# Optimization experiments

Hardware: AMD Instinct MI355X
Metric: run time of the kernel (lower is better)

The kernel has to match this reference:

```python
import jax, jax.numpy as jnp
import numpy as np


def setup_inputs() -> dict:
    key = jax.random.key(0)
    k1, k2, k3 = jax.random.split(key, 3)
    return {
        "x": jax.random.normal(k1, (1, 64, 28, 28), dtype=jnp.float32),
        "w1": jax.random.normal(k2, (128, 32, 3, 3, 2), dtype=jnp.float32),  # weights[0]
        "w2": jax.random.normal(k3, (64, 3, 2), dtype=jnp.float32),          # weights[1]
    }


def reference(x, w1, w2):
    # Stage 1: first unfold + einsum == depthwise size-3 conv along W (pad 1),
    # producing 2 taps (k) per channel.
    xr = x.reshape(64, 28, 28)                      # (j, m=H, n=W)
    xp = jnp.pad(xr, ((0, 0), (0, 0), (1, 1)))      # zero-pad W by 1
    # t3[j, m, i, n] = xp[j, m, n + i]  (i = kernel offset 0..2)
    t3 = jnp.stack([xp[:, :, i:i + 28] for i in range(3)], axis=2)  # (64,28,3,28)
    t4 = jnp.einsum('jmin,jik->jmnk', t3, w2)       # (64,28,28,2)

    # Stage 2: pairwise channel-sum 64 -> 32
    t5 = t4.reshape(32, 2, 28, 28, 2).sum(axis=1)   # (l=32, h=28, w=28, k=2)

    # Stage 3: the two remaining unfolds + final einsum == standard 3x3 conv,
    # pad 1, in_channels = (l,k) = 64, out_channels = 128.
    inp = jnp.transpose(t5, (0, 3, 1, 2)).reshape(1, 64, 28, 28)       # NCHW, C=(l,k)
    w = jnp.transpose(w1, (0, 1, 4, 2, 3)).reshape(128, 64, 3, 3)      # OIHW, I=(l,m)
    y = jax.lax.conv_general_dilated(
        inp, w, window_strides=(1, 1), padding=((1, 1), (1, 1)),
        dimension_numbers=('NCHW', 'OIHW', 'NCHW'))
    return y  # (1, 128, 28, 28)
```

## Files before the change

### kernel.cpp

```cpp
#include <hip/hip_runtime.h>
#include <hip/hip_bf16.h>

__global__ __launch_bounds__(256, 2) void fused_kernel(
    const float* __restrict__ x,
    const float* __restrict__ w1,
    const float* __restrict__ w2,
    float* __restrict__ y)
{
    __shared__ __align__(16) float sA[64 * 220];

    const int b     = blockIdx.x;
    const int opair = b / 7;
    const int band  = b % 7;
    const int tid   = threadIdx.x;

    for (int task = tid; task < 384; task += 256) {
        const int c  = task / 6;
        const int pr = task % 6;
        const int m  = band * 4 + pr - 1;
        float* dst = &sA[c * 220 + pr * 36];
        if (m < 0 || m > 27) {
            #pragma unroll
            for (int t = 0; t < 7; ++t)
                ((float4*)dst)[t] = make_float4(0.f, 0.f, 0.f, 0.f);
            ((float2*)dst)[14] = make_float2(0.f, 0.f);
        } else {
            const int j0 = c & ~1;
            const int k  = c & 1;
            const float* xr0 = x + (j0 * 28 + m) * 28;
            const float* xr1 = xr0 + 28 * 28;
            const float* w2p = w2 + j0 * 6 + k;
            const float wa0 = w2p[0], wa1 = w2p[2],  wa2 = w2p[4];
            const float wb0 = w2p[6], wb1 = w2p[8],  wb2 = w2p[10];

            float4 pv0 = make_float4(0.f, 0.f, 0.f, 0.f);
            float4 pv1 = make_float4(0.f, 0.f, 0.f, 0.f);
            #pragma unroll
            for (int t = 0; t < 7; ++t) {
                float4 v0 = ((const float4*)xr0)[t];
                float4 v1 = ((const float4*)xr1)[t];
                float4 o;
                o.x = wa0 * pv0.z + wa1 * pv0.w + wa2 * v0.x
                    + wb0 * pv1.z + wb1 * pv1.w + wb2 * v1.x;
                o.y = wa0 * pv0.w + wa1 * v0.x + wa2 * v0.y
                    + wb0 * pv1.w + wb1 * v1.x + wb2 * v1.y;
                o.z = wa0 * v0.x + wa1 * v0.y + wa2 * v0.z
                    + wb0 * v1.x + wb1 * v1.y + wb2 * v1.z;
                o.w = wa0 * v0.y + wa1 * v0.z + wa2 * v0.w
                    + wb0 * v1.y + wb1 * v1.z + wb2 * v1.w;
                if (t == 0) o.x = 0.f;
                ((float4*)dst)[t] = o;
                pv0 = v0; pv1 = v1;
            }
            float t28 = wa0 * pv0.z + wa1 * pv0.w
                      + wb0 * pv1.z + wb1 * pv1.w;
            ((float2*)dst)[14] = make_float2(t28, 0.f);
        }
    }
    __syncthreads();

    const int oo    = tid >> 7;
    const int r     = tid & 127;
    const int c4    = r & 3;
    const int strip = r >> 2;
    const bool act  = (strip < 28);
    const int sclp  = act ? strip : 0;
    const int dh    = sclp / 7;
    const int st    = sclp % 7;
    const int o     = opair * 2 + oo;

    float acc0 = 0.f, acc1 = 0.f, acc2 = 0.f, acc3 = 0.f;
    const float* wbo = w1 + o * 576;

    #pragma unroll 2
    for (int li = 0; li < 8; ++li) {
        const int l = c4 + li * 4;
        const float* w9 = wbo + l * 18;
        const float* rowA = &sA[(2 * l) * 220 + dh * 36 + st * 4];
        #pragma unroll
        for (int dy = 0; dy < 3; ++dy) {
            float2 ws0 = *(const float2*)(w9 + dy * 6 + 0);
            float2 ws1 = *(const float2*)(w9 + dy * 6 + 2);
            float2 ws2 = *(const float2*)(w9 + dy * 6 + 4);
            const float* rA = rowA + dy * 36;
            const float* rB = rA + 220;
            float4 a  = *(const float4*)rA;
            float2 a2 = *(const float2*)(rA + 4);
            float4 bb = *(const float4*)rB;
            float2 b2 = *(const float2*)(rB + 4);

            acc0 += ws0.x * a.x  + ws1.x * a.y  + ws2.x * a.z
                  + ws0.y * bb.x + ws1.y * bb.y + ws2.y * bb.z;
            acc1 += ws0.x * a.y  + ws1.x * a.z  + ws2.x * a.w
                  + ws0.y * bb.y + ws1.y * bb.z + ws2.y * bb.w;
            acc2 += ws0.x * a.z  + ws1.x * a.w  + ws2.x * a2.x
                  + ws0.y * bb.z + ws1.y * bb.w + ws2.y * b2.x;
            acc3 += ws0.x * a.w  + ws1.x * a2.x + ws2.x * a2.y
                  + ws0.y * bb.w + ws1.y * b2.x + ws2.y * b2.y;
        }
    }

    acc0 += __shfl_xor(acc0, 1); acc1 += __shfl_xor(acc1, 1);
    acc2 += __shfl_xor(acc2, 1); acc3 += __shfl_xor(acc3, 1);
    acc0 += __shfl_xor(acc0, 2); acc1 += __shfl_xor(acc1, 2);
    acc2 += __shfl_xor(acc2, 2); acc3 += __shfl_xor(acc3, 2);

    if (act && c4 == 0) {
        const int R = band * 4 + dh;
        float* yp = y + (o * 28 + R) * 28 + st * 4;
        *(float4*)yp = make_float4(acc0, acc1, acc2, acc3);
    }
}

extern "C" void kernel_launch(void* const* d_in, const int* in_sizes, int n_in,
                              void* d_out, int out_size, void* d_ws, size_t ws_size,
                              hipStream_t stream) {
    const float* x  = (const float*)d_in[0];
    const float* w1 = (const float*)d_in[1];
    const float* w2 = (const float*)d_in[2];
    float* yout = (float*)d_out;

    fused_kernel<<<dim3(448), dim3(256), 0, stream>>>(x, w1, w2, yout);
}
```

Baseline: 14.71 us.

## Compute two output rows per thread with register-cached conv weights

Reworks the conv stage's thread mapping. Each thread now splits the channel reduction eight ways and computes two adjacent output rows, so every shared-memory row it loads feeds both rows. All 36 weight float2 values a thread needs are preloaded into registers before the stage-1 pass, so the global weight loads overlap the depthwise stage. This cuts LDS traffic and weight reloads, at the cost of higher register pressure with launch bounds of 2 blocks, and an extra shuffle-reduction step.

```diff
diff --git a/kernel.cpp b/kernel.cpp
--- a/kernel.cpp
+++ b/kernel.cpp
@@ -13,6 +13,26 @@
     const int opair = b / 7;
     const int band  = b % 7;
     const int tid   = threadIdx.x;
+
+    const int l8      = tid & 7;
+    const int strip   = tid >> 3;
+    const bool act    = (strip < 28);
+    const int sclp    = act ? strip : 0;
+    const int oo      = sclp / 14;
+    const int rem     = sclp % 14;
+    const int rp      = rem / 7;
+    const int st      = rem % 7;
+    const int o       = opair * 2 + oo;
+
+    float2 wreg[4][9];
+    {
+        const float* wb = w1 + o * 576 + l8 * 18;
+        #pragma unroll
+        for (int li = 0; li < 4; ++li)
+            #pragma unroll
+            for (int t = 0; t < 9; ++t)
+                wreg[li][t] = *(const float2*)(wb + li * 144 + t * 2);
+    }
 
     for (int task = tid; task < 384; task += 256) {
         const int c  = task / 6;
@@ -39,17 +59,17 @@
             for (int t = 0; t < 7; ++t) {
                 float4 v0 = ((const float4*)xr0)[t];
                 float4 v1 = ((const float4*)xr1)[t];
-                float4 o;
-                o.x = wa0 * pv0.z + wa1 * pv0.w + wa2 * v0.x
-                    + wb0 * pv1.z + wb1 * pv1.w + wb2 * v1.x;
-                o.y = wa0 * pv0.w + wa1 * v0.x + wa2 * v0.y
-                    + wb0 * pv1.w + wb1 * v1.x + wb2 * v1.y;
-                o.z = wa0 * v0.x + wa1 * v0.y + wa2 * v0.z
-                    + wb0 * v1.x + wb1 * v1.y + wb2 * v1.z;
-                o.w = wa0 * v0.y + wa1 * v0.z + wa2 * v0.w
-                    + wb0 * v1.y + wb1 * v1.z + wb2 * v1.w;
-                if (t == 0) o.x = 0.f;
-                ((float4*)dst)[t] = o;
+                float4 ov;
+                ov.x = wa0 * pv0.z + wa1 * pv0.w + wa2 * v0.x
+                     + wb0 * pv1.z + wb1 * pv1.w + wb2 * v1.x;
+                ov.y = wa0 * pv0.w + wa1 * v0.x + wa2 * v0.y
+                     + wb0 * pv1.w + wb1 * v1.x + wb2 * v1.y;
+                ov.z = wa0 * v0.x + wa1 * v0.y + wa2 * v0.z
+                     + wb0 * v1.x + wb1 * v1.y + wb2 * v1.z;
+                ov.w = wa0 * v0.y + wa1 * v0.z + wa2 * v0.w
+                     + wb0 * v1.y + wb1 * v1.z + wb2 * v1.w;
+                if (t == 0) ov.x = 0.f;
+                ((float4*)dst)[t] = ov;
                 pv0 = v0; pv1 = v1;
             }
             float t28 = wa0 * pv0.z + wa1 * pv0.w
@@ -59,56 +79,60 @@
     }
     __syncthreads();
 
-    const int oo    = tid >> 7;
-    const int r     = tid & 127;
-    const int c4    = r & 3;
-    const int strip = r >> 2;
-    const bool act  = (strip < 28);
-    const int sclp  = act ? strip : 0;
-    const int dh    = sclp / 7;
-    const int st    = sclp % 7;
-    const int o     = opair * 2 + oo;
+    float acc00 = 0.f, acc01 = 0.f, acc02 = 0.f, acc03 = 0.f;
+    float acc10 = 0.f, acc11 = 0.f, acc12 = 0.f, acc13 = 0.f;
 
-    float acc0 = 0.f, acc1 = 0.f, acc2 = 0.f, acc3 = 0.f;
-    const float* wbo = w1 + o * 576;
-
-    #pragma unroll 2
-    for (int li = 0; li < 8; ++li) {
-        const int l = c4 + li * 4;
-        const float* w9 = wbo + l * 18;
-        const float* rowA = &sA[(2 * l) * 220 + dh * 36 + st * 4];
+    #pragma unroll
+    for (int li = 0; li < 4; ++li) {
         #pragma unroll
-        for (int dy = 0; dy < 3; ++dy) {
-            float2 ws0 = *(const float2*)(w9 + dy * 6 + 0);
-            float2 ws1 = *(const float2*)(w9 + dy * 6 + 2);
-            float2 ws2 = *(const float2*)(w9 + dy * 6 + 4);
-            const float* rA = rowA + dy * 36;
-            const float* rB = rA + 220;
-            float4 a  = *(const float4*)rA;
-            float2 a2 = *(const float2*)(rA + 4);
-            float4 bb = *(const float4*)rB;
-            float2 b2 = *(const float2*)(rB + 4);
-
-            acc0 += ws0.x * a.x  + ws1.x * a.y  + ws2.x * a.z
-                  + ws0.y * bb.x + ws1.y * bb.y + ws2.y * bb.z;
-            acc1 += ws0.x * a.y  + ws1.x * a.z  + ws2.x * a.w
-                  + ws0.y * bb.y + ws1.y * bb.z + ws2.y * bb.w;
-            acc2 += ws0.x * a.z  + ws1.x * a.w  + ws2.x * a2.x
-                  + ws0.y * bb.z + ws1.y * bb.w + ws2.y * b2.x;
-            acc3 += ws0.x * a.w  + ws1.x * a2.x + ws2.x * a2.y
-                  + ws0.y * bb.w + ws1.y * b2.x + ws2.y * b2.y;
+        for (int ch = 0; ch < 2; ++ch) {
+            const int c = (l8 + li * 8) * 2 + ch;
+            const float* sa = &sA[c * 220 + (rp * 2) * 36 + st * 4];
+            #pragma unroll
+            for (int q = 0; q < 4; ++q) {
+                float4 t0 = *(const float4*)(sa + q * 36);
+                float2 t1 = *(const float2*)(sa + q * 36 + 4);
+                if (q < 3) {
+                    float2 W0 = wreg[li][q * 3 + 0];
+                    float2 W1 = wreg[li][q * 3 + 1];
+                    float2 W2 = wreg[li][q * 3 + 2];
+                    float wa = ch ? W0.y : W0.x;
+                    float wbv = ch ? W1.y : W1.x;
+                    float wc = ch ? W2.y : W2.x;
+                    acc00 += wa * t0.x + wbv * t0.y + wc * t0.z;
+                    acc01 += wa * t0.y + wbv * t0.z + wc * t0.w;
+                    acc02 += wa * t0.z + wbv * t0.w + wc * t1.x;
+                    acc03 += wa * t0.w + wbv * t1.x + wc * t1.y;
+                }
+                if (q >= 1) {
+                    float2 W0 = wreg[li][(q - 1) * 3 + 0];
+                    float2 W1 = wreg[li][(q - 1) * 3 + 1];
+                    float2 W2 = wreg[li][(q - 1) * 3 + 2];
+                    float wa = ch ? W0.y : W0.x;
+                    float wbv = ch ? W1.y : W1.x;
+                    float wc = ch ? W2.y : W2.x;
+                    acc10 += wa * t0.x + wbv * t0.y + wc * t0.z;
+                    acc11 += wa * t0.y + wbv * t0.z + wc * t0.w;
+                    acc12 += wa * t0.z + wbv * t0.w + wc * t1.x;
+                    acc13 += wa * t0.w + wbv * t1.x + wc * t1.y;
+                }
+            }
         }
     }
 
-    acc0 += __shfl_xor(acc0, 1); acc1 += __shfl_xor(acc1, 1);
-    acc2 += __shfl_xor(acc2, 1); acc3 += __shfl_xor(acc3, 1);
-    acc0 += __shfl_xor(acc0, 2); acc1 += __shfl_xor(acc1, 2);
-    acc2 += __shfl_xor(acc2, 2); acc3 += __shfl_xor(acc3, 2);
+    #pragma unroll
+    for (int m = 1; m <= 4; m <<= 1) {
+        acc00 += __shfl_xor(acc00, m); acc01 += __shfl_xor(acc01, m);
+        acc02 += __shfl_xor(acc02, m); acc03 += __shfl_xor(acc03, m);
+        acc10 += __shfl_xor(acc10, m); acc11 += __shfl_xor(acc11, m);
+        acc12 += __shfl_xor(acc12, m); acc13 += __shfl_xor(acc13, m);
+    }
 
-    if (act && c4 == 0) {
-        const int R = band * 4 + dh;
-        float* yp = y + (o * 28 + R) * 28 + st * 4;
-        *(float4*)yp = make_float4(acc0, acc1, acc2, acc3);
+    if (act && l8 == 0) {
+        const int R0 = band * 4 + rp * 2;
+        float* yp = y + (o * 28 + R0) * 28 + st * 4;
+        *(float4*)yp        = make_float4(acc00, acc01, acc02, acc03);
+        *(float4*)(yp + 28) = make_float4(acc10, acc11, acc12, acc13);
     }
 }
 
```

Measured after the change: 14.63 us. About the same (-0.5%).
